# Kernel optimization log

Measured on AMD Instinct MI355X. Metric: run time of the kernel, lower is better.

The kernel has to match this reference:

```python
import jax, jax.numpy as jnp
import numpy as np

N_HEAD = 16
MASK_VALUE = -10000.0


def setup_inputs() -> dict:
    key = jax.random.key(0)
    ks = jax.random.split(key, 5)
    B, S, D = 2, 2048, 1024
    return {
        "x": jax.random.normal(ks[0], (B, S, D), dtype=jnp.float32),
        "qkv_w": jax.random.normal(ks[1], (D, 3 * D), dtype=jnp.float32) * 0.02,
        "qkv_b": jnp.zeros((3 * D,), dtype=jnp.float32),
        "proj_w": jax.random.normal(ks[2], (D, D), dtype=jnp.float32) * 0.02,
        "proj_b": jnp.zeros((D,), dtype=jnp.float32),
    }


def reference(x, qkv_w, qkv_b, proj_w, proj_b):
    B, S, D = x.shape
    H = N_HEAD
    hd = D // H

    # fused QKV projection, then split (torch.split along last dim)
    qkv = x @ qkv_w + qkv_b                      # [B, S, 3D]
    q, k, v = jnp.split(qkv, 3, axis=-1)

    def split_heads(t):  # [B, S, D] -> [B, H, S, hd]
        return t.reshape(B, S, H, hd).transpose(0, 2, 1, 3)

    q, k, v = split_heads(q), split_heads(k), split_heads(v)

    # scaled dot-product scores (scale_attn_weights=True)
    scores = jnp.einsum("bhqd,bhkd->bhqk", q, k) / jnp.sqrt(jnp.asarray(hd, x.dtype))

    # causal mask: tril over [query_len, key_len] (no cache, so q_len == k_len == S)
    causal = jnp.tril(jnp.ones((S, S), dtype=bool))[None, None]
    scores = jnp.where(causal, scores, jnp.asarray(MASK_VALUE, x.dtype))

    attn = jax.nn.softmax(scores, axis=-1)       # dropout p=0 (eval): identity
    out = jnp.einsum("bhqk,bhkd->bhqd", attn, v)

    # merge heads and output projection (resid dropout p=0)
    out = out.transpose(0, 2, 1, 3).reshape(B, S, D)
    out = out @ proj_w + proj_b
    return out
```

## Files before the change

kernel.cpp:

```cpp
#include <hip/hip_runtime.h>
#include <hip/hip_bf16.h>


#define SEQ 2048
#define DM 1024
#define HD 64
#define NHEAD 16
#define BHTOT 32

typedef unsigned short u16;
typedef __bf16 bf16_t;
typedef bf16_t bf16x8 __attribute__((ext_vector_type(8)));
typedef float f32x4 __attribute__((ext_vector_type(4)));
typedef float f32x16 __attribute__((ext_vector_type(16)));

__device__ __forceinline__ u16 f2bf(float f) {
  unsigned u = __float_as_uint(f);
  u += 0x7fffu + ((u >> 16) & 1u);
  return (u16)(u >> 16);
}

__device__ __forceinline__ f32x4 mfma16(uint4 a, uint4 b, f32x4 c) {
  return __builtin_amdgcn_mfma_f32_16x16x32_bf16(
      __builtin_bit_cast(bf16x8, a), __builtin_bit_cast(bf16x8, b), c, 0, 0, 0);
}

__device__ __forceinline__ f32x16 mfma32(uint4 a, uint4 b, f32x16 c) {
  return __builtin_amdgcn_mfma_f32_32x32x16_bf16(
      __builtin_bit_cast(bf16x8, a), __builtin_bit_cast(bf16x8, b), c, 0, 0, 0);
}

__device__ __forceinline__ unsigned cvtpk(float lo, float hi) {
  unsigned d;
  asm("v_cvt_pk_bf16_f32 %0, %1, %2" : "=v"(d) : "v"(lo), "v"(hi));
  return d;
}

__device__ __forceinline__ void gload_lds16(const u16* g, void* l) {
  __builtin_amdgcn_global_load_lds(
      (const __attribute__((address_space(1))) unsigned*)g,
      (__attribute__((address_space(3))) unsigned*)l, 16, 0, 0);
}

__device__ __forceinline__ void ttile(const float* __restrict__ W,
                                      u16* __restrict__ Wt, int K, int N,
                                      int n0, int k0) {
  __shared__ u16 t[32][132];
  const int tid = threadIdx.x;
  const int tx = tid & 31, ty = tid >> 5;
#pragma unroll
  for (int i = 0; i < 4; ++i) {
    const int k = ty + i * 8;
    float4 v = *(const float4*)(W + (size_t)(k0 + k) * N + n0 + tx * 4);
    t[k][tx * 4 + 0] = f2bf(v.x);
    t[k][tx * 4 + 1] = f2bf(v.y);
    t[k][tx * 4 + 2] = f2bf(v.z);
    t[k][tx * 4 + 3] = f2bf(v.w);
  }
  __syncthreads();
  const int n = tid >> 1, half = tid & 1;
  u16 tmp[16];
#pragma unroll
  for (int j = 0; j < 16; ++j) tmp[j] = t[half * 16 + j][n];
  uint4 lo, hi;
  lo.x = (unsigned)tmp[0] | ((unsigned)tmp[1] << 16);
  lo.y = (unsigned)tmp[2] | ((unsigned)tmp[3] << 16);
  lo.z = (unsigned)tmp[4] | ((unsigned)tmp[5] << 16);
  lo.w = (unsigned)tmp[6] | ((unsigned)tmp[7] << 16);
  hi.x = (unsigned)tmp[8] | ((unsigned)tmp[9] << 16);
  hi.y = (unsigned)tmp[10] | ((unsigned)tmp[11] << 16);
  hi.z = (unsigned)tmp[12] | ((unsigned)tmp[13] << 16);
  hi.w = (unsigned)tmp[14] | ((unsigned)tmp[15] << 16);
  u16* base = Wt + (size_t)(n0 + n) * K + k0 + half * 16;
  *(uint4*)base = lo;
  *(uint4*)(base + 8) = hi;
}

__global__ __launch_bounds__(256) void prep(
    const float* __restrict__ x, const float* __restrict__ wqkv,
    const float* __restrict__ wproj, u16* __restrict__ xb,
    u16* __restrict__ wqkvT, u16* __restrict__ wprojT) {
  const int bid = blockIdx.x;
  if (bid < 4096) {
    int i = (bid * 256 + threadIdx.x) * 4;
    float4 v = *(const float4*)(x + i);
    uint2 pk;
    pk.x = (unsigned)f2bf(v.x) | ((unsigned)f2bf(v.y) << 16);
    pk.y = (unsigned)f2bf(v.z) | ((unsigned)f2bf(v.w) << 16);
    *(uint2*)(xb + i) = pk;
  } else if (bid < 4096 + 768) {
    const int tb = bid - 4096;
    const int nt = tb % 24, kt = tb / 24;
    ttile(wqkv, wqkvT, DM, 3072, nt * 128, kt * 32);
  } else {
    const int tb = bid - 4864;
    const int nt = tb & 7, kt = tb >> 3;
    ttile(wproj, wprojT, DM, DM, nt * 128, kt * 32);
  }
}

__global__ __launch_bounds__(256) void qkv_gemm(
    const u16* __restrict__ A, const u16* __restrict__ Bt,
    const float* __restrict__ bias,
    u16* __restrict__ qb, u16* __restrict__ kb, u16* __restrict__ vb) {
  __shared__ u16 Al[128 * 64];
  __shared__ u16 Bl[128 * 64];
  const int tid = threadIdx.x;
  const int m0 = blockIdx.y * 128;
  const int n0 = blockIdx.x * 128;
  const int w = tid >> 6, lane = tid & 63;
  const int lr = lane & 15, lg = lane >> 4;
  const int wm = (w >> 1) * 64, wn = (w & 1) * 64;
  const int Kd = DM;
  const int srow = lane >> 3;
  const int scol = ((lane & 7) ^ srow) << 3;

  f32x4 acc[4][4] = {};

  for (int kk = 0; kk < Kd; kk += 64) {
    __syncthreads();
#pragma unroll
    for (int i = 0; i < 4; ++i) {
      const int c = i * 4 + w;
      const int row = c * 8 + srow;
      gload_lds16(A + (size_t)(m0 + row) * Kd + kk + scol, (char*)Al + c * 1024);
      gload_lds16(Bt + (size_t)(n0 + row) * Kd + kk + scol, (char*)Bl + c * 1024);
    }
    __syncthreads();
#pragma unroll
    for (int h2 = 0; h2 < 2; ++h2) {
      const int sl = (((h2 * 4 + lg) ^ (lr & 7)) << 3);
      uint4 af[4], bfr[4];
#pragma unroll
      for (int mi = 0; mi < 4; ++mi)
        af[mi] = *(const uint4*)(Al + (wm + mi * 16 + lr) * 64 + sl);
#pragma unroll
      for (int ni = 0; ni < 4; ++ni)
        bfr[ni] = *(const uint4*)(Bl + (wn + ni * 16 + lr) * 64 + sl);
#pragma unroll
      for (int mi = 0; mi < 4; ++mi)
#pragma unroll
        for (int ni = 0; ni < 4; ++ni)
          acc[mi][ni] = mfma16(af[mi], bfr[ni], acc[mi][ni]);
    }
  }

#pragma unroll
  for (int mi = 0; mi < 4; ++mi) {
#pragma unroll
    for (int ni = 0; ni < 4; ++ni) {
      const int n = n0 + wn + ni * 16 + lr;
      const float bv = bias[n];
      const int part = n >> 10;
      const int d = n & 1023;
      const int h = d >> 6, dim = d & 63;
      const int m_base = m0 + wm + mi * 16 + lg * 4;
      const int b = m_base >> 11, s = m_base & 2047;
      const int bh = b * NHEAD + h;
      if (part == 0) {
        u16* p = qb + ((size_t)bh * SEQ + s) * HD + dim;
#pragma unroll
        for (int r = 0; r < 4; ++r)
          p[r * HD] = f2bf((acc[mi][ni][r] + bv) * 0.18033688f);
      } else if (part == 1) {
        u16* p = kb + ((size_t)bh * SEQ + s) * HD + dim;
#pragma unroll
        for (int r = 0; r < 4; ++r) p[r * HD] = f2bf(acc[mi][ni][r] + bv);
      } else {
        const int sx = ((((s >> 2) ^ (s >> 3)) & 1) ? (s ^ 12) : s);
        uint2 pk;
        pk.x = (unsigned)f2bf(acc[mi][ni][0] + bv) |
               ((unsigned)f2bf(acc[mi][ni][1] + bv) << 16);
        pk.y = (unsigned)f2bf(acc[mi][ni][2] + bv) |
               ((unsigned)f2bf(acc[mi][ni][3] + bv) << 16);
        *(uint2*)(vb + ((size_t)bh * HD + dim) * SEQ + sx) = pk;
      }
    }
  }
}

__global__ __launch_bounds__(128) void attn_kernel(
    const u16* __restrict__ Q, const u16* __restrict__ K,
    const u16* __restrict__ Vt, u16* __restrict__ O) {
  const int lane = threadIdx.x & 63;
  const int w = threadIdx.x >> 6;
  const int r31 = lane & 31;
  const int hi = lane >> 5;
  const int bh = blockIdx.x & 31;
  const int j = 31 - (blockIdx.x >> 5);
  const int qt = 2 * j + w;
  const int q0w = qt * 32;
  const int nst = j + 1;

  const u16* Qb = Q + (size_t)bh * SEQ * HD;
  const u16* Kb = K + (size_t)bh * SEQ * HD;
  const u16* Vb = Vt + (size_t)bh * HD * SEQ;

  uint4 qf[4];
#pragma unroll
  for (int ks = 0; ks < 4; ++ks)
    qf[ks] = *(const uint4*)(Qb + (size_t)(q0w + r31) * HD + ks * 16 + hi * 8);

  f32x16 ot0 = {}, ot1 = {};
  float L = 0.f;

#define LOADK(KF, kv0)                                                          \
  {                                                                             \
    _Pragma("unroll") for (int ks = 0; ks < 4; ++ks) {                          \
      KF[ks] = *(const uint4*)(Kb + (size_t)((kv0) + r31) * HD + ks * 16 + hi * 8); \
      KF[ks + 4] =                                                              \
          *(const uint4*)(Kb + (size_t)((kv0) + 32 + r31) * HD + ks * 16 + hi * 8); \
    }                                                                           \
  }

#define RELAYOUT(dst, S, base)                                                  \
  {                                                                             \
    dst.x = cvtpk(S[base + 0], S[base + 1]);                                    \
    dst.y = cvtpk(S[base + 2], S[base + 3]);                                    \
    dst.z = cvtpk(S[base + 4], S[base + 5]);                                    \
    dst.w = cvtpk(S[base + 6], S[base + 7]);                                    \
  }

#define STEP(KF, KN)                                                            \
  {                                                                             \
    const int kv0 = t << 6;                                                     \
    const bool last = (t == nst - 1);                                           \
    const bool skip1 = last && ((qt & 1) == 0);   \
    uint4 vf[8];                                                                \
    _Pragma("unroll") for (int ks = 0; ks < 2; ++ks) {                          \
      vf[ks] = *(const uint4*)(Vb + (size_t)r31 * SEQ + kv0 + ks * 16 + hi * 8); \
      vf[ks + 4] =                                                              \
          *(const uint4*)(Vb + (size_t)(32 + r31) * SEQ + kv0 + ks * 16 + hi * 8); \
    }                                                                           \
    if (!skip1) {                                                               \
      _Pragma("unroll") for (int ks = 2; ks < 4; ++ks) {                        \
        vf[ks] = *(const uint4*)(Vb + (size_t)r31 * SEQ + kv0 + ks * 16 + hi * 8); \
        vf[ks + 4] =                                                            \
            *(const uint4*)(Vb + (size_t)(32 + r31) * SEQ + kv0 + ks * 16 + hi * 8); \
      }                                                                         \
    }                                                                           \
    f32x16 s0 = {}, s1 = {};                                                    \
    _Pragma("unroll") for (int ks = 0; ks < 4; ++ks)                            \
        s0 = mfma32(KF[ks], qf[ks], s0);                                        \
    if (!skip1) {                                                               \
      _Pragma("unroll") for (int ks = 0; ks < 4; ++ks)                          \
          s1 = mfma32(KF[ks + 4], qf[ks], s1);                                  \
    }                                                                           \
    if (t + 1 < nst) LOADK(KN, kv0 + 64);                                       \
    if (last) {                                                                 \
      _Pragma("unroll") for (int i = 0; i < 16; ++i) {                          \
        const int row = (i & 3) + 8 * (i >> 2) + 4 * hi;                        \
        if (skip1) {                                                            \
          if (row > r31) s0[i] = -1e30f;                                        \
        } else {                                                                \
          if (row > r31) s1[i] = -1e30f;                                        \
        }                                                                       \
      }                                                                         \
    }                                                                           \
    float rs = 0.f;                                                             \
    _Pragma("unroll") for (int i = 0; i < 16; ++i) {                            \
      s0[i] = __builtin_exp2f(s0[i]);                                           \
      rs += s0[i];                                                              \
    }                                                                           \
    if (!skip1) {                                                               \
      _Pragma("unroll") for (int i = 0; i < 16; ++i) {                          \
        s1[i] = __builtin_exp2f(s1[i]);                                         \
        rs += s1[i];                                                            \
      }                                                                         \
    }                                                                           \
    L += rs;                                                                    \
    uint4 pa[4];                                                                \
    RELAYOUT(pa[0], s0, 0);                                                     \
    RELAYOUT(pa[1], s0, 8);                                                     \
    if (!skip1) {                                                               \
      RELAYOUT(pa[2], s1, 0);                                                   \
      RELAYOUT(pa[3], s1, 8);                                                   \
    }                                                                           \
    _Pragma("unroll") for (int ks = 0; ks < 2; ++ks) {                          \
      ot0 = mfma32(vf[ks], pa[ks], ot0);                                        \
      ot1 = mfma32(vf[ks + 4], pa[ks], ot1);                                    \
    }                                                                           \
    if (!skip1) {                                                               \
      _Pragma("unroll") for (int ks = 2; ks < 4; ++ks) {                        \
        ot0 = mfma32(vf[ks], pa[ks], ot0);                                      \
        ot1 = mfma32(vf[ks + 4], pa[ks], ot1);                                  \
      }                                                                         \
    }                                                                           \
  }

  uint4 kA[8], kB[8];
  LOADK(kA, 0);
  int t = 0;
  for (;;) {
    STEP(kA, kB);
    if (++t >= nst) break;
    STEP(kB, kA);
    if (++t >= nst) break;
  }
#undef STEP
#undef RELAYOUT
#undef LOADK

  L += __shfl_xor(L, 32);
  const float inv = 1.0f / L;
  const int b = bh >> 4, h = bh & 15;
  u16* Orow = O + ((size_t)b * SEQ + q0w + r31) * DM + h * HD;
#pragma unroll
  for (int g = 0; g < 4; ++g) {
    uint2 p0, p1;
    p0.x = (unsigned)f2bf(ot0[4 * g + 0] * inv) | ((unsigned)f2bf(ot0[4 * g + 1] * inv) << 16);
    p0.y = (unsigned)f2bf(ot0[4 * g + 2] * inv) | ((unsigned)f2bf(ot0[4 * g + 3] * inv) << 16);
    p1.x = (unsigned)f2bf(ot1[4 * g + 0] * inv) | ((unsigned)f2bf(ot1[4 * g + 1] * inv) << 16);
    p1.y = (unsigned)f2bf(ot1[4 * g + 2] * inv) | ((unsigned)f2bf(ot1[4 * g + 3] * inv) << 16);
    *(uint2*)(Orow + 8 * g + 4 * hi) = p0;
    *(uint2*)(Orow + 32 + 8 * g + 4 * hi) = p1;
  }
}

__global__ __launch_bounds__(256) void proj_gemm(
    const u16* __restrict__ A, const u16* __restrict__ Bt,
    const float* __restrict__ bias, float* __restrict__ out) {
  __shared__ u16 Al[128 * 64];
  __shared__ u16 Bl[64 * 64];
  const int tid = threadIdx.x;
  const int m0 = blockIdx.y * 128;
  const int n0 = blockIdx.x * 64;
  const int w = tid >> 6, lane = tid & 63;
  const int lr = lane & 15, lg = lane >> 4;
  const int wm = w * 32;
  const int Kd = DM;
  const int srow = lane >> 3;
  const int scol = ((lane & 7) ^ srow) << 3;

  f32x4 acc[2][4] = {};

  for (int kk = 0; kk < Kd; kk += 64) {
    __syncthreads();
#pragma unroll
    for (int i = 0; i < 4; ++i) {
      const int c = i * 4 + w;
      const int row = c * 8 + srow;
      gload_lds16(A + (size_t)(m0 + row) * Kd + kk + scol, (char*)Al + c * 1024);
    }
#pragma unroll
    for (int i = 0; i < 2; ++i) {
      const int c = i * 4 + w;
      const int row = c * 8 + srow;
      gload_lds16(Bt + (size_t)(n0 + row) * Kd + kk + scol, (char*)Bl + c * 1024);
    }
    __syncthreads();
#pragma unroll
    for (int h2 = 0; h2 < 2; ++h2) {
      const int sl = (((h2 * 4 + lg) ^ (lr & 7)) << 3);
      uint4 af[2], bfr[4];
#pragma unroll
      for (int mi = 0; mi < 2; ++mi)
        af[mi] = *(const uint4*)(Al + (wm + mi * 16 + lr) * 64 + sl);
#pragma unroll
      for (int ni = 0; ni < 4; ++ni)
        bfr[ni] = *(const uint4*)(Bl + (ni * 16 + lr) * 64 + sl);
#pragma unroll
      for (int mi = 0; mi < 2; ++mi)
#pragma unroll
        for (int ni = 0; ni < 4; ++ni)
          acc[mi][ni] = mfma16(af[mi], bfr[ni], acc[mi][ni]);
    }
  }

#pragma unroll
  for (int mi = 0; mi < 2; ++mi)
#pragma unroll
    for (int ni = 0; ni < 4; ++ni)
#pragma unroll
      for (int r = 0; r < 4; ++r) {
        int m = m0 + wm + mi * 16 + lg * 4 + r;
        int n = n0 + ni * 16 + lr;
        out[(size_t)m * DM + n] = acc[mi][ni][r] + bias[n];
      }
}

extern "C" void kernel_launch(void* const* d_in, const int* in_sizes, int n_in,
                              void* d_out, int out_size, void* d_ws, size_t ws_size,
                              hipStream_t stream) {
  const float* x      = (const float*)d_in[0];
  const float* qkv_w  = (const float*)d_in[1];
  const float* qkv_b  = (const float*)d_in[2];
  const float* proj_w = (const float*)d_in[3];
  const float* proj_b = (const float*)d_in[4];
  float* out = (float*)d_out;

  const size_t per = (size_t)BHTOT * SEQ * HD;
  u16* qb = (u16*)d_ws;
  u16* kb = qb + per;
  u16* vb = kb + per;
  u16* xb = vb + per;
  u16* ab = xb;
  u16* wqkvT = xb + (size_t)SEQ * 2 * DM;
  u16* wprojT = wqkvT + (size_t)3072 * DM;

  dim3 blk(256);
  prep<<<dim3(5120), blk, 0, stream>>>(x, qkv_w, proj_w, xb, wqkvT, wprojT);
  qkv_gemm<<<dim3(24, 32), blk, 0, stream>>>(xb, wqkvT, qkv_b, qb, kb, vb);
  attn_kernel<<<dim3(1024), dim3(128), 0, stream>>>(qb, kb, vb, ab);
  proj_gemm<<<dim3(16, 32), blk, 0, stream>>>(ab, wprojT, proj_b, out);
}
```

Before: 140.5 us.

## Process two query tiles per wave to reuse K/V fragments in attention

Each wave now handles two adjacent 32-row query tiles (64 queries) of one head instead of one. The K and V fragments loaded from global memory are shared by both tiles, which halves the K/V load traffic per query and lets the score MFMAs of the second tile interleave with the softmax of the first. Two waves in a block now cover different heads, and the grid is halved. In exchange, register pressure rises (twice the Q fragments and accumulators) and K is no longer double-buffered, so the load of the next K tile has less latency hiding and occupancy may drop.

```diff
diff --git a/kernel.cpp b/kernel.cpp
--- a/kernel.cpp
+++ b/kernel.cpp
@@ -186,23 +186,25 @@
   const int w = threadIdx.x >> 6;
   const int r31 = lane & 31;
   const int hi = lane >> 5;
-  const int bh = blockIdx.x & 31;
-  const int j = 31 - (blockIdx.x >> 5);
-  const int qt = 2 * j + w;
-  const int q0w = qt * 32;
-  const int nst = j + 1;
+  const int m = 31 - (blockIdx.x >> 4);
+  const int bh = ((blockIdx.x & 15) << 1) | w;
+  const int q0a = m * 64;
+  const int q0b = m * 64 + 32;
+  const int nst = m + 1;
 
   const u16* Qb = Q + (size_t)bh * SEQ * HD;
   const u16* Kb = K + (size_t)bh * SEQ * HD;
   const u16* Vb = Vt + (size_t)bh * HD * SEQ;
 
-  uint4 qf[4];
-#pragma unroll
-  for (int ks = 0; ks < 4; ++ks)
-    qf[ks] = *(const uint4*)(Qb + (size_t)(q0w + r31) * HD + ks * 16 + hi * 8);
-
-  f32x16 ot0 = {}, ot1 = {};
-  float L = 0.f;
+  uint4 qfa[4], qfb[4];
+#pragma unroll
+  for (int ks = 0; ks < 4; ++ks) {
+    qfa[ks] = *(const uint4*)(Qb + (size_t)(q0a + r31) * HD + ks * 16 + hi * 8);
+    qfb[ks] = *(const uint4*)(Qb + (size_t)(q0b + r31) * HD + ks * 16 + hi * 8);
+  }
+
+  f32x16 oa0 = {}, oa1 = {}, ob0 = {}, ob1 = {};
+  float La = 0.f, Lb = 0.f;
 
 #define LOADK(KF, kv0)                                                          \
   {                                                                             \
@@ -221,99 +223,130 @@
     dst.w = cvtpk(S[base + 6], S[base + 7]);                                    \
   }
 
-#define STEP(KF, KN)                                                            \
-  {                                                                             \
-    const int kv0 = t << 6;                                                     \
-    const bool last = (t == nst - 1);                                           \
-    const bool skip1 = last && ((qt & 1) == 0);   \
-    uint4 vf[8];                                                                \
-    _Pragma("unroll") for (int ks = 0; ks < 2; ++ks) {                          \
-      vf[ks] = *(const uint4*)(Vb + (size_t)r31 * SEQ + kv0 + ks * 16 + hi * 8); \
-      vf[ks + 4] =                                                              \
-          *(const uint4*)(Vb + (size_t)(32 + r31) * SEQ + kv0 + ks * 16 + hi * 8); \
-    }                                                                           \
-    if (!skip1) {                                                               \
-      _Pragma("unroll") for (int ks = 2; ks < 4; ++ks) {                        \
-        vf[ks] = *(const uint4*)(Vb + (size_t)r31 * SEQ + kv0 + ks * 16 + hi * 8); \
-        vf[ks + 4] =                                                            \
-            *(const uint4*)(Vb + (size_t)(32 + r31) * SEQ + kv0 + ks * 16 + hi * 8); \
-      }                                                                         \
-    }                                                                           \
-    f32x16 s0 = {}, s1 = {};                                                    \
-    _Pragma("unroll") for (int ks = 0; ks < 4; ++ks)                            \
-        s0 = mfma32(KF[ks], qf[ks], s0);                                        \
-    if (!skip1) {                                                               \
-      _Pragma("unroll") for (int ks = 0; ks < 4; ++ks)                          \
-          s1 = mfma32(KF[ks + 4], qf[ks], s1);                                  \
-    }                                                                           \
-    if (t + 1 < nst) LOADK(KN, kv0 + 64);                                       \
-    if (last) {                                                                 \
-      _Pragma("unroll") for (int i = 0; i < 16; ++i) {                          \
-        const int row = (i & 3) + 8 * (i >> 2) + 4 * hi;                        \
-        if (skip1) {                                                            \
-          if (row > r31) s0[i] = -1e30f;                                        \
-        } else {                                                                \
-          if (row > r31) s1[i] = -1e30f;                                        \
-        }                                                                       \
-      }                                                                         \
-    }                                                                           \
-    float rs = 0.f;                                                             \
-    _Pragma("unroll") for (int i = 0; i < 16; ++i) {                            \
-      s0[i] = __builtin_exp2f(s0[i]);                                           \
-      rs += s0[i];                                                              \
-    }                                                                           \
-    if (!skip1) {                                                               \
-      _Pragma("unroll") for (int i = 0; i < 16; ++i) {                          \
-        s1[i] = __builtin_exp2f(s1[i]);                                         \
-        rs += s1[i];                                                            \
-      }                                                                         \
-    }                                                                           \
-    L += rs;                                                                    \
-    uint4 pa[4];                                                                \
-    RELAYOUT(pa[0], s0, 0);                                                     \
-    RELAYOUT(pa[1], s0, 8);                                                     \
-    if (!skip1) {                                                               \
-      RELAYOUT(pa[2], s1, 0);                                                   \
-      RELAYOUT(pa[3], s1, 8);                                                   \
-    }                                                                           \
-    _Pragma("unroll") for (int ks = 0; ks < 2; ++ks) {                          \
-      ot0 = mfma32(vf[ks], pa[ks], ot0);                                        \
-      ot1 = mfma32(vf[ks + 4], pa[ks], ot1);                                    \
-    }                                                                           \
-    if (!skip1) {                                                               \
-      _Pragma("unroll") for (int ks = 2; ks < 4; ++ks) {                        \
-        ot0 = mfma32(vf[ks], pa[ks], ot0);                                      \
-        ot1 = mfma32(vf[ks + 4], pa[ks], ot1);                                  \
-      }                                                                         \
-    }                                                                           \
-  }
-
-  uint4 kA[8], kB[8];
-  LOADK(kA, 0);
-  int t = 0;
-  for (;;) {
-    STEP(kA, kB);
-    if (++t >= nst) break;
-    STEP(kB, kA);
-    if (++t >= nst) break;
-  }
-#undef STEP
+  uint4 kf[8];
+  LOADK(kf, 0);
+
+  for (int t = 0; t < nst; ++t) {
+    const int kv0 = t << 6;
+    const bool last = (t == nst - 1);
+    uint4 vf[8];
+#pragma unroll
+    for (int ks = 0; ks < 4; ++ks) {
+      vf[ks] = *(const uint4*)(Vb + (size_t)r31 * SEQ + kv0 + ks * 16 + hi * 8);
+      vf[ks + 4] = *(const uint4*)(Vb + (size_t)(32 + r31) * SEQ + kv0 + ks * 16 + hi * 8);
+    }
+    f32x16 sa0 = {}, sa1 = {};
+#pragma unroll
+    for (int ks = 0; ks < 4; ++ks) sa0 = mfma32(kf[ks], qfa[ks], sa0);
+    if (!last) {
+#pragma unroll
+      for (int ks = 0; ks < 4; ++ks) sa1 = mfma32(kf[ks + 4], qfa[ks], sa1);
+    }
+    if (last) {
+#pragma unroll
+      for (int i = 0; i < 16; ++i) {
+        const int row = (i & 3) + 8 * (i >> 2) + 4 * hi;
+        if (row > r31) sa0[i] = -1e30f;
+      }
+    }
+    {
+      float rs = 0.f;
+#pragma unroll
+      for (int i = 0; i < 16; ++i) {
+        sa0[i] = __builtin_exp2f(sa0[i]);
+        rs += sa0[i];
+      }
+      if (!last) {
+#pragma unroll
+        for (int i = 0; i < 16; ++i) {
+          sa1[i] = __builtin_exp2f(sa1[i]);
+          rs += sa1[i];
+        }
+      }
+      La += rs;
+    }
+    uint4 pa[4];
+    RELAYOUT(pa[0], sa0, 0);
+    RELAYOUT(pa[1], sa0, 8);
+    if (!last) {
+      RELAYOUT(pa[2], sa1, 0);
+      RELAYOUT(pa[3], sa1, 8);
+    }
+    f32x16 sb0 = {}, sb1 = {};
+#pragma unroll
+    for (int ks = 0; ks < 4; ++ks) sb0 = mfma32(kf[ks], qfb[ks], sb0);
+#pragma unroll
+    for (int ks = 0; ks < 4; ++ks) sb1 = mfma32(kf[ks + 4], qfb[ks], sb1);
+    if (t + 1 < nst) LOADK(kf, kv0 + 64);
+#pragma unroll
+    for (int ks = 0; ks < 2; ++ks) {
+      oa0 = mfma32(vf[ks], pa[ks], oa0);
+      oa1 = mfma32(vf[ks + 4], pa[ks], oa1);
+    }
+    if (!last) {
+#pragma unroll
+      for (int ks = 2; ks < 4; ++ks) {
+        oa0 = mfma32(vf[ks], pa[ks], oa0);
+        oa1 = mfma32(vf[ks + 4], pa[ks], oa1);
+      }
+    }
+    if (last) {
+#pragma unroll
+      for (int i = 0; i < 16; ++i) {
+        const int row = (i & 3) + 8 * (i >> 2) + 4 * hi;
+        if (row > r31) sb1[i] = -1e30f;
+      }
+    }
+    {
+      float rs = 0.f;
+#pragma unroll
+      for (int i = 0; i < 16; ++i) {
+        sb0[i] = __builtin_exp2f(sb0[i]);
+        rs += sb0[i];
+      }
+#pragma unroll
+      for (int i = 0; i < 16; ++i) {
+        sb1[i] = __builtin_exp2f(sb1[i]);
+        rs += sb1[i];
+      }
+      Lb += rs;
+    }
+    uint4 pb[4];
+    RELAYOUT(pb[0], sb0, 0);
+    RELAYOUT(pb[1], sb0, 8);
+    RELAYOUT(pb[2], sb1, 0);
+    RELAYOUT(pb[3], sb1, 8);
+#pragma unroll
+    for (int ks = 0; ks < 4; ++ks) {
+      ob0 = mfma32(vf[ks], pb[ks], ob0);
+      ob1 = mfma32(vf[ks + 4], pb[ks], ob1);
+    }
+  }
 #undef RELAYOUT
 #undef LOADK
 
-  L += __shfl_xor(L, 32);
-  const float inv = 1.0f / L;
+  La += __shfl_xor(La, 32);
+  Lb += __shfl_xor(Lb, 32);
+  const float inva = 1.0f / La, invb = 1.0f / Lb;
   const int b = bh >> 4, h = bh & 15;
-  u16* Orow = O + ((size_t)b * SEQ + q0w + r31) * DM + h * HD;
+  u16* OrowA = O + ((size_t)b * SEQ + q0a + r31) * DM + h * HD;
+  u16* OrowB = O + ((size_t)b * SEQ + q0b + r31) * DM + h * HD;
 #pragma unroll
   for (int g = 0; g < 4; ++g) {
     uint2 p0, p1;
-    p0.x = (unsigned)f2bf(ot0[4 * g + 0] * inv) | ((unsigned)f2bf(ot0[4 * g + 1] * inv) << 16);
-    p0.y = (unsigned)f2bf(ot0[4 * g + 2] * inv) | ((unsigned)f2bf(ot0[4 * g + 3] * inv) << 16);
-    p1.x = (unsigned)f2bf(ot1[4 * g + 0] * inv) | ((unsigned)f2bf(ot1[4 * g + 1] * inv) << 16);
-    p1.y = (unsigned)f2bf(ot1[4 * g + 2] * inv) | ((unsigned)f2bf(ot1[4 * g + 3] * inv) << 16);
-    *(uint2*)(Orow + 8 * g + 4 * hi) = p0;
-    *(uint2*)(Orow + 32 + 8 * g + 4 * hi) = p1;
+    p0.x = (unsigned)f2bf(oa0[4 * g + 0] * inva) | ((unsigned)f2bf(oa0[4 * g + 1] * inva) << 16);
+    p0.y = (unsigned)f2bf(oa0[4 * g + 2] * inva) | ((unsigned)f2bf(oa0[4 * g + 3] * inva) << 16);
+    p1.x = (unsigned)f2bf(oa1[4 * g + 0] * inva) | ((unsigned)f2bf(oa1[4 * g + 1] * inva) << 16);
+    p1.y = (unsigned)f2bf(oa1[4 * g + 2] * inva) | ((unsigned)f2bf(oa1[4 * g + 3] * inva) << 16);
+    *(uint2*)(OrowA + 8 * g + 4 * hi) = p0;
+    *(uint2*)(OrowA + 32 + 8 * g + 4 * hi) = p1;
+    uint2 q0_, q1_;
+    q0_.x = (unsigned)f2bf(ob0[4 * g + 0] * invb) | ((unsigned)f2bf(ob0[4 * g + 1] * invb) << 16);
+    q0_.y = (unsigned)f2bf(ob0[4 * g + 2] * invb) | ((unsigned)f2bf(ob0[4 * g + 3] * invb) << 16);
+    q1_.x = (unsigned)f2bf(ob1[4 * g + 0] * invb) | ((unsigned)f2bf(ob1[4 * g + 1] * invb) << 16);
+    q1_.y = (unsigned)f2bf(ob1[4 * g + 2] * invb) | ((unsigned)f2bf(ob1[4 * g + 3] * invb) << 16);
+    *(uint2*)(OrowB + 8 * g + 4 * hi) = q0_;
+    *(uint2*)(OrowB + 32 + 8 * g + 4 * hi) = q1_;
   }
 }
 
@@ -401,6 +434,6 @@
   dim3 blk(256);
   prep<<<dim3(5120), blk, 0, stream>>>(x, qkv_w, proj_w, xb, wqkvT, wprojT);
   qkv_gemm<<<dim3(24, 32), blk, 0, stream>>>(xb, wqkvT, qkv_b, qb, kb, vb);
-  attn_kernel<<<dim3(1024), dim3(128), 0, stream>>>(qb, kb, vb, ab);
+  attn_kernel<<<dim3(512), dim3(128), 0, stream>>>(qb, kb, vb, ab);
   proj_gemm<<<dim3(16, 32), blk, 0, stream>>>(ab, wprojT, proj_b, out);
 }
```

New measurement: 141.9 us. About the same (+1.0%).
